# Kernel optimization log

Measured on AMD Instinct MI355X. Metric: run time of the kernel, lower is better.

The kernel has to match this reference:

```python
import jax, jax.numpy as jnp
import numpy as np

EPS = 1e-5

def _conv(x, w, b):
    # stride-2, pad-1 3x3 conv, NCHW / OIHW
    y = jax.lax.conv_general_dilated(x, w, (2, 2), [(1, 1), (1, 1)],
                                     dimension_numbers=('NCHW', 'OIHW', 'NCHW'))
    return y + b[None, :, None, None]

def _bn(x, gamma, beta):
    # training-mode batchnorm: batch statistics over (N,H,W), biased variance
    mu = x.mean(axis=(0, 2, 3), keepdims=True)
    var = x.var(axis=(0, 2, 3), keepdims=True)
    return gamma[None, :, None, None] * (x - mu) * jax.lax.rsqrt(var + EPS) + beta[None, :, None, None]

def setup_inputs():
    key = jax.random.key(0)
    ks = iter(jax.random.split(key, 40))
    def rn(shape, scale=0.05):
        return jax.random.normal(next(ks), shape, dtype=jnp.float32) * scale
    d = {}
    d['img'] = jax.random.normal(next(ks), (64, 3, 75, 75), dtype=jnp.float32)
    d['qst'] = jax.random.normal(next(ks), (64, 11), dtype=jnp.float32)
    # conv stack 3->32->64->128->256
    d['w1'] = rn((32, 3, 3, 3));    d['b1'] = jnp.zeros((32,), jnp.float32)
    d['w2'] = rn((64, 32, 3, 3));   d['b2'] = jnp.zeros((64,), jnp.float32)
    d['w3'] = rn((128, 64, 3, 3));  d['b3'] = jnp.zeros((128,), jnp.float32)
    d['w4'] = rn((256, 128, 3, 3)); d['b4'] = jnp.zeros((256,), jnp.float32)
    for i, c in zip((1, 2, 3, 4), (32, 64, 128, 256)):
        d[f'g{i}'] = jnp.ones((c,), jnp.float32)
        d[f'be{i}'] = jnp.zeros((c,), jnp.float32)
    # g MLP (torch Linear weights are [out,in])
    d['gw1'] = rn((2000, 523)); d['gb1'] = jnp.zeros((2000,), jnp.float32)
    d['gw2'] = rn((2000, 2000)); d['gb2'] = jnp.zeros((2000,), jnp.float32)
    d['gw3'] = rn((2000, 2000)); d['gb3'] = jnp.zeros((2000,), jnp.float32)
    d['gw4'] = rn((2000, 2000)); d['gb4'] = jnp.zeros((2000,), jnp.float32)
    # f MLP
    d['fw1'] = rn((1000, 2000)); d['fb1'] = jnp.zeros((1000,), jnp.float32)
    d['fw2'] = rn((500, 1000));  d['fb2'] = jnp.zeros((500,), jnp.float32)
    d['fw3'] = rn((100, 500));   d['fb3'] = jnp.zeros((100,), jnp.float32)
    d['fw4'] = rn((10, 100));    d['fb4'] = jnp.zeros((10,), jnp.float32)
    return d

def reference(img, qst, w1, b1, w2, b2, w3, b3, w4, b4,
              g1, be1, g2, be2, g3, be3, g4, be4,
              gw1, gb1, gw2, gb2, gw3, gb3, gw4, gb4,
              fw1, fb1, fw2, fb2, fw3, fb3, fw4, fb4):
    x = jax.nn.relu(_bn(_conv(img, w1, b1), g1, be1))
    x = jax.nn.relu(_bn(_conv(x, w2, b2), g2, be2))
    x = jax.nn.relu(_bn(_conv(x, w3, b3), g3, be3))
    x = jax.nn.relu(_bn(_conv(x, w4, b4), g4, be4))   # [B,256,5,5]
    B = x.shape[0]
    obj = x.reshape(B, 256, 25).transpose(0, 2, 1)     # [B,25,256], row-major like the loop
    oi = jnp.broadcast_to(obj[:, :, None, :], (B, 25, 25, 256))
    oj = jnp.broadcast_to(obj[:, None, :, :], (B, 25, 25, 256))
    q = jnp.broadcast_to(qst[:, None, None, :], (B, 25, 25, 11))
    pairs = jnp.concatenate([oi, oj, q], axis=-1).reshape(B * 625, 523)
    h = jax.nn.relu(pairs @ gw1.T + gb1)
    h = jax.nn.relu(h @ gw2.T + gb2)
    h = jax.nn.relu(h @ gw3.T + gb3)
    h = jax.nn.relu(h @ gw4.T + gb4)
    x_g = h.reshape(B, 625, 2000).sum(axis=1) / 625.0
    x_f = jax.nn.relu(x_g @ fw1.T + fb1)
    x_f = jax.nn.relu(x_f @ fw2.T + fb2)
    x_f = jax.nn.relu(x_f @ fw3.T + fb3)
    x_f = x_f @ fw4.T + fb4
    return jax.nn.log_softmax(x_f, axis=-1)
```

## Files before the change

### kernel.cpp

```cpp
#include <hip/hip_runtime.h>

typedef unsigned short u16;
typedef unsigned int u32;
typedef __attribute__((ext_vector_type(8))) short bf16x8;
typedef __attribute__((ext_vector_type(4))) float f32x4;

#define BN_EPS 1e-5f
#define BN_S 16

__device__ __forceinline__ float bf2f(u16 u) {
  union { unsigned u; float f; } x; x.u = ((unsigned)u) << 16; return x.f;
}
__device__ __forceinline__ u16 f2bf(float f) {
  union { float f; unsigned u; } x; x.f = f;
  unsigned r = x.u + 0x7FFFu + ((x.u >> 16) & 1u);
  return (u16)(r >> 16);
}

__global__ __launch_bounds__(256) void conv1_lds(const float* __restrict__ img,
                                                 const float* __restrict__ w,
                                                 const float* __restrict__ b,
                                                 float* __restrict__ C1) {
  int blk = blockIdx.x;
  int n = blk / 38, ho = blk % 38;
  __shared__ float in_s[9 * 80];
  __shared__ float w_s[32 * 27];
  __shared__ float b_s[32];
  int t = threadIdx.x;
  for (int i = t; i < 720; i += 256) in_s[i] = 0.f;
  __syncthreads();
  for (int i = t; i < 675; i += 256) {
    int wi = i % 75; int q = i / 75; int kh = q % 3; int ci = q / 3;
    int hi = ho * 2 - 1 + kh;
    if (hi >= 0 && hi < 75)
      in_s[(ci * 3 + kh) * 80 + wi + 1] = img[((size_t)(n * 3 + ci) * 75 + hi) * 75 + wi];
  }
  for (int i = t; i < 864; i += 256) w_s[i] = w[i];
  if (t < 32) b_s[t] = b[t];
  __syncthreads();
  for (int idx = t; idx < 1216; idx += 256) {
    int wo = idx >> 5, co = idx & 31;
    float acc = b_s[co];
    const float* wp = w_s + co * 27;
#pragma unroll
    for (int ci = 0; ci < 3; ci++) {
#pragma unroll
      for (int kh = 0; kh < 3; kh++) {
        const float* ip = in_s + (ci * 3 + kh) * 80 + 2 * wo;
        const float* wq = wp + ci * 9 + kh * 3;
        acc += ip[0] * wq[0] + ip[1] * wq[1] + ip[2] * wq[2];
      }
    }
    C1[((size_t)blk * 38 + wo) * 32 + co] = acc;
  }
}

__global__ void bn_partial(const float* __restrict__ C, int ldc, int M,
                           float* __restrict__ part) {
  int c = blockIdx.x; int s = blockIdx.y; int t = threadIdx.x;
  int rowsPer = (M + BN_S - 1) / BN_S;
  int r0 = s * rowsPer; int r1 = r0 + rowsPer; if (r1 > M) r1 = M;
  float s1 = 0.f, s2 = 0.f;
  for (int r = r0 + t; r < r1; r += 256) {
    float v = C[(size_t)r * ldc + c]; s1 += v; s2 += v * v;
  }
  __shared__ float l1[256], l2[256];
  l1[t] = s1; l2[t] = s2; __syncthreads();
  for (int off = 128; off > 0; off >>= 1) {
    if (t < off) { l1[t] += l1[t + off]; l2[t] += l2[t + off]; }
    __syncthreads();
  }
  if (t == 0) { part[s * 512 + c] = l1[0]; part[s * 512 + 256 + c] = l2[0]; }
}

__global__ void bn_final(const float* __restrict__ part, const float* __restrict__ gamma,
                         const float* __restrict__ beta, float* __restrict__ ss,
                         int C, int M) {
  int c = threadIdx.x;
  if (c >= C) { if (c < 256) { ss[c] = 0.f; ss[256 + c] = 0.f; } return; }
  float s1 = 0.f, s2 = 0.f;
#pragma unroll
  for (int s = 0; s < BN_S; s++) { s1 += part[s * 512 + c]; s2 += part[s * 512 + 256 + c]; }
  float mu = s1 / M;
  float var = s2 / M - mu * mu;
  float sc = gamma[c] * rsqrtf(var + BN_EPS);
  ss[c] = sc; ss[256 + c] = beta[c] - mu * sc;
}

__global__ void bnrelu_im2col(const float* __restrict__ Cprev, int ldprev, int Hp, int Wp,
                              const float* __restrict__ ss, u16* __restrict__ X,
                              int Ho, int Wo, int Ci, int Mp) {
  int civ4 = Ci >> 2;
  int idx = blockIdx.x * blockDim.x + threadIdx.x;
  int total = Mp * 9 * civ4;
  if (idx >= total) return;
  int cv = idx % civ4; int t2 = idx / civ4;
  int tap = t2 % 9; int row = t2 / 9;
  int K = 9 * Ci;
  u16* dst = X + (size_t)row * K + tap * Ci + cv * 4;
  int HW = Ho * Wo;
  int Mvalid = 64 * HW;
  ushort4 o4; o4.x = 0; o4.y = 0; o4.z = 0; o4.w = 0;
  if (row < Mvalid) {
    int wo = row % Wo; int t = row / Wo;
    int ho = t % Ho; int n = t / Ho;
    int kh = tap / 3, kw = tap % 3;
    int hi = ho * 2 - 1 + kh, wi = wo * 2 - 1 + kw;
    if (hi >= 0 && hi < Hp && wi >= 0 && wi < Wp) {
      const float* src = Cprev + ((size_t)((n * Hp + hi) * Wp + wi)) * ldprev + cv * 4;
      float4 v = *(const float4*)src;
      int c0 = cv * 4;
      float a;
      a = v.x * ss[c0 + 0] + ss[256 + c0 + 0]; o4.x = f2bf(a > 0.f ? a : 0.f);
      a = v.y * ss[c0 + 1] + ss[256 + c0 + 1]; o4.y = f2bf(a > 0.f ? a : 0.f);
      a = v.z * ss[c0 + 2] + ss[256 + c0 + 2]; o4.z = f2bf(a > 0.f ? a : 0.f);
      a = v.w * ss[c0 + 3] + ss[256 + c0 + 3]; o4.w = f2bf(a > 0.f ? a : 0.f);
    }
  }
  *(ushort4*)dst = o4;
}

__global__ void pack_convw(const float* __restrict__ w, u16* __restrict__ Wp,
                           int Co, int Ci, int Cop) {
  int K = 9 * Ci;
  int idx = blockIdx.x * blockDim.x + threadIdx.x;
  if (idx >= Cop * K) return;
  int k = idx % K; int co = idx / K;
  int tap = k / Ci; int ci = k % Ci;
  float v = (co < Co) ? w[((size_t)co * Ci + ci) * 9 + tap] : 0.f;
  Wp[idx] = f2bf(v);
}

__global__ void pad_bias(const float* __restrict__ b, float* __restrict__ bc, int Co, int Cop) {
  int i = blockIdx.x * blockDim.x + threadIdx.x;
  if (i < Cop) bc[i] = (i < Co) ? b[i] : 0.f;
}

__global__ void obj_from_c4(const float* __restrict__ C4, const float* __restrict__ ss,
                            u16* __restrict__ obj) {
  int idx = blockIdx.x * blockDim.x + threadIdx.x;
  if (idx >= 1664 * 256) return;
  int c = idx & 255; int row = idx >> 8;
  float v = 0.f;
  if (row < 1600) {
    float x = C4[(size_t)row * 256 + c];
    x = x * ss[c] + ss[256 + c];
    v = x > 0.f ? x : 0.f;
  }
  obj[idx] = f2bf(v);
}

__global__ void pack_w1(const float* __restrict__ gw1, u16* __restrict__ W1a, u16* __restrict__ W1b) {
  int idx = blockIdx.x * blockDim.x + threadIdx.x;
  if (idx >= 2048 * 256) return;
  int k = idx & 255, n = idx >> 8;
  float a = 0.f, b = 0.f;
  if (n < 2000) { a = gw1[(size_t)n * 523 + k]; b = gw1[(size_t)n * 523 + 256 + k]; }
  W1a[idx] = f2bf(a); W1b[idx] = f2bf(b);
}

__global__ void pack_wpad(const float* __restrict__ w, u16* __restrict__ Wp,
                          int N, int K, int Np, int Kp) {
  int idx = blockIdx.x * blockDim.x + threadIdx.x;
  if (idx >= Np * Kp) return;
  int k = idx % Kp, n = idx / Kp;
  float v = (n < N && k < K) ? w[(size_t)n * K + k] : 0.f;
  Wp[idx] = f2bf(v);
}

__global__ void pack_bias3(const float* __restrict__ b2, const float* __restrict__ b3,
                           const float* __restrict__ b4, float* __restrict__ bp) {
  int i = blockIdx.x * blockDim.x + threadIdx.x;
  if (i >= 2048) return;
  bp[i]        = (i < 2000) ? b2[i] : 0.f;
  bp[2048 + i] = (i < 2000) ? b3[i] : 0.f;
  bp[4096 + i] = (i < 2000) ? b4[i] : 0.f;
}

__global__ void q_build(const float* __restrict__ qst, const float* __restrict__ gw1,
                        const float* __restrict__ gb1, float* __restrict__ Q) {
  int idx = blockIdx.x * blockDim.x + threadIdx.x;
  if (idx >= 64 * 2048) return;
  int o = idx & 2047, b = idx >> 11;
  float v = 0.f;
  if (o < 2000) {
    v = gb1[o];
    const float* w = gw1 + (size_t)o * 523 + 512;
    const float* q = qst + b * 11;
#pragma unroll
    for (int k = 0; k < 11; k++) v += q[k] * w[k];
  }
  Q[idx] = v;
}

__global__ void pack_xgb(const float* __restrict__ xg, u16* __restrict__ xgb) {
  int idx = blockIdx.x * blockDim.x + threadIdx.x;
  if (idx >= 128 * 2048) return;
  int row = idx >> 11;
  float v = (row < 64) ? xg[idx] * (1.f / 625.f) : 0.f;
  xgb[idx] = f2bf(v);
}

typedef const __attribute__((address_space(1))) u32* gas1;
typedef __attribute__((address_space(3))) u32* las3;
__device__ __forceinline__ void gld16(const void* g, void* l) {
  __builtin_amdgcn_global_load_lds((gas1)g, (las3)l, 16, 0, 0);
}

template <int EPI>
__global__ __launch_bounds__(256) void gemm_bt(
    const u16* __restrict__ A, int lda,
    const u16* __restrict__ W, int ldb,
    float* __restrict__ Cf, u16* __restrict__ Cb, int ldc,
    const float* __restrict__ bias, int KT, int NTN) {
  __shared__ __align__(16) char lds[32768];
  int bid = blockIdx.x;
  int wg;
  if ((gridDim.x & 7) == 0) {
    int cpx = gridDim.x >> 3;
    wg = (bid & 7) * cpx + (bid >> 3);
  } else {
    wg = bid;
  }
  int mt = wg / NTN, nt = wg % NTN;
  int tid = threadIdx.x;
  int wave = tid >> 6, lane = tid & 63;
  int r = lane & 15, g = lane >> 4;
  int wr = wave >> 1, wc = wave & 1;

  const u16* Asrc = A + (size_t)(mt * 128 + wave * 32 + r) * lda + g * 8;
  const u16* Wsrc = W + (size_t)(nt * 128 + wave * 32 + r) * ldb + g * 8;

  f32x4 acc[4][4];
#pragma unroll
  for (int i = 0; i < 4; i++)
#pragma unroll
    for (int j = 0; j < 4; j++) acc[i][j] = (f32x4){0.f, 0.f, 0.f, 0.f};

  {
    char* Al = lds; char* Wl = lds + 8192;
    gld16(Asrc, Al + wave * 2048);
    gld16(Asrc + (size_t)16 * lda, Al + wave * 2048 + 1024);
    gld16(Wsrc, Wl + wave * 2048);
    gld16(Wsrc + (size_t)16 * ldb, Wl + wave * 2048 + 1024);
  }
  __syncthreads();

  int buf = 0;
  for (int kt = 0; kt < KT; kt++) {
    if (kt + 1 < KT) {
      int k0 = (kt + 1) * 32;
      char* Al = lds + (buf ^ 1) * 16384; char* Wl = Al + 8192;
      gld16(Asrc + k0, Al + wave * 2048);
      gld16(Asrc + k0 + (size_t)16 * lda, Al + wave * 2048 + 1024);
      gld16(Wsrc + k0, Wl + wave * 2048);
      gld16(Wsrc + k0 + (size_t)16 * ldb, Wl + wave * 2048 + 1024);
    }
    char* Al = lds + buf * 16384; char* Wl = Al + 8192;
    bf16x8 a[4], w[4];
#pragma unroll
    for (int i = 0; i < 4; i++) a[i] = *(const bf16x8*)(Al + (wr * 4 + i) * 1024 + lane * 16);
#pragma unroll
    for (int j = 0; j < 4; j++) w[j] = *(const bf16x8*)(Wl + (wc * 4 + j) * 1024 + lane * 16);
#pragma unroll
    for (int i = 0; i < 4; i++)
#pragma unroll
      for (int j = 0; j < 4; j++)
        acc[i][j] = __builtin_amdgcn_mfma_f32_16x16x32_bf16(a[i], w[j], acc[i][j], 0, 0, 0);
    __syncthreads();
    buf ^= 1;
  }

  int rowb = mt * 128 + wr * 64 + (lane >> 4) * 4;
  int colb = nt * 128 + wc * 64 + (lane & 15);
#pragma unroll
  for (int i = 0; i < 4; i++) {
#pragma unroll
    for (int j = 0; j < 4; j++) {
      int col = colb + j * 16;
      float bv = (EPI == 2 || EPI == 5) ? bias[col] : 0.f;
#pragma unroll
      for (int q = 0; q < 4; q++) {
        int row = rowb + i * 16 + q;
        float v = acc[i][j][q];
        if (EPI == 2) {
          Cf[(size_t)row * ldc + col] = v + bv;
        } else if (EPI == 3) {
          Cb[(size_t)row * ldc + col] = f2bf(v);
        } else if (EPI == 5) {
          float z = v + bv; z = z > 0.f ? z : 0.f;
          Cb[(size_t)row * ldc + col] = f2bf(z);
        } else {
          Cf[(size_t)row * ldc + col] = v;
        }
      }
    }
  }
}

#define MF16(d, av, bv) d = __builtin_amdgcn_mfma_f32_16x16x32_bf16(av, bv, d, 0, 0, 0)

template <int NT, int SUM>
__global__ __launch_bounds__(512, 2) void gemm256(
    const u16* __restrict__ A, const u16* __restrict__ W,
    u16* __restrict__ Cb, const float* __restrict__ bias,
    float* __restrict__ rp4, int r0c, int nvalid) {
  __shared__ __align__(16) char lds[131072];
  int bid = blockIdx.x;
  int cpx = gridDim.x >> 3;
  int wg = (bid & 7) * cpx + (bid >> 3);
  int mt = wg >> 3, nt = wg & 7;
  int tid = threadIdx.x;
  int wave = tid >> 6, lane = tid & 63;
  int wr = wave >> 2, wc = wave & 3;
  int wcl = wc & 1, wch = wc >> 1;
  int l15 = lane & 15, l7 = lane & 7, lh = lane >> 4;

  int srcChunkOff = (((lane & 7) ^ (lane >> 3)) << 3);
  int srcRowInWave = (lane >> 3);
  auto stageA = [&](int tt, int slot, int h) {
#pragma unroll
    for (int s = 0; s < 2; s++) {
      const u16* src = A + (size_t)(mt * 256 + h * 128 + s * 64 + wave * 8 + srcRowInWave) * 2048
                         + tt * 64 + srcChunkOff;
      gld16(src, lds + slot * 65536 + h * 16384 + s * 8192 + wave * 1024);
    }
  };
  auto stageB = [&](int tt, int slot, int h) {
#pragma unroll
    for (int s = 0; s < 2; s++) {
      const u16* src = W + (size_t)(nt * 256 + h * 128 + s * 64 + wave * 8 + srcRowInWave) * 2048
                         + tt * 64 + srcChunkOff;
      gld16(src, lds + slot * 65536 + 32768 + h * 16384 + s * 8192 + wave * 1024);
    }
  };

  f32x4 acc[8][4];
#pragma unroll
  for (int i = 0; i < 8; i++)
#pragma unroll
    for (int j = 0; j < 4; j++) acc[i][j] = (f32x4){0.f, 0.f, 0.f, 0.f};

  stageA(0, 0, 0); stageA(0, 0, 1); stageB(0, 0, 0); stageB(0, 0, 1);
  stageB(1, 1, 0); stageB(1, 1, 1);
  asm volatile("s_waitcnt vmcnt(4)" ::: "memory");
  __builtin_amdgcn_s_barrier();

  bf16x8 b00, b01, b10, b11, b20, b21, b30, b31;

#define AROFF(Q, i, ks) \
  ((((2 * (Q) + (i)) * 16 + l15) * 128) + (((((ks) * 4) + lh) ^ l7) << 4))
#define BROFF(j, ks) \
  ((((wcl * 4 + (j)) * 16 + l15) * 128) + (((((ks) * 4) + lh) ^ l7) << 4))

#define PHASE(Q, T, BUF)                                                         \
  {                                                                              \
    const char* Ab = lds + (BUF) * 65536 + wr * 16384;                           \
    const char* Bb = lds + (BUF) * 65536 + 32768 + wch * 16384;                  \
    if (Q == 0) {                                                                \
      b00 = *(const bf16x8*)(Bb + BROFF(0, 0));                                  \
      b01 = *(const bf16x8*)(Bb + BROFF(0, 1));                                  \
      b10 = *(const bf16x8*)(Bb + BROFF(1, 0));                                  \
      b11 = *(const bf16x8*)(Bb + BROFF(1, 1));                                  \
      b20 = *(const bf16x8*)(Bb + BROFF(2, 0));                                  \
      b21 = *(const bf16x8*)(Bb + BROFF(2, 1));                                  \
      b30 = *(const bf16x8*)(Bb + BROFF(3, 0));                                  \
      b31 = *(const bf16x8*)(Bb + BROFF(3, 1));                                  \
    }                                                                            \
    bf16x8 a00 = *(const bf16x8*)(Ab + AROFF(Q, 0, 0));                          \
    bf16x8 a01 = *(const bf16x8*)(Ab + AROFF(Q, 0, 1));                          \
    bf16x8 a10 = *(const bf16x8*)(Ab + AROFF(Q, 1, 0));                          \
    bf16x8 a11 = *(const bf16x8*)(Ab + AROFF(Q, 1, 1));                          \
    if (Q == 0) { if ((T) + 1 < NT) stageA((T) + 1, (BUF) ^ 1, 0); }             \
    if (Q == 1) { if ((T) + 1 < NT) stageA((T) + 1, (BUF) ^ 1, 1);               \
                  if ((T) + 2 < NT) stageB((T) + 2, (BUF), 0); }                 \
    if (Q == 2) { if ((T) + 2 < NT) stageB((T) + 2, (BUF), 1); }                 \
    __builtin_amdgcn_s_barrier();                                                \
    __builtin_amdgcn_s_setprio(1);                                               \
    MF16(acc[2 * Q + 0][0], a00, b00); MF16(acc[2 * Q + 0][0], a01, b01);        \
    MF16(acc[2 * Q + 0][1], a00, b10); MF16(acc[2 * Q + 0][1], a01, b11);        \
    MF16(acc[2 * Q + 0][2], a00, b20); MF16(acc[2 * Q + 0][2], a01, b21);        \
    MF16(acc[2 * Q + 0][3], a00, b30); MF16(acc[2 * Q + 0][3], a01, b31);        \
    MF16(acc[2 * Q + 1][0], a10, b00); MF16(acc[2 * Q + 1][0], a11, b01);        \
    MF16(acc[2 * Q + 1][1], a10, b10); MF16(acc[2 * Q + 1][1], a11, b11);        \
    MF16(acc[2 * Q + 1][2], a10, b20); MF16(acc[2 * Q + 1][2], a11, b21);        \
    MF16(acc[2 * Q + 1][3], a10, b30); MF16(acc[2 * Q + 1][3], a11, b31);        \
    __builtin_amdgcn_s_setprio(0);                                               \
    if (Q == 3) { asm volatile("s_waitcnt vmcnt(4)" ::: "memory"); }             \
    __builtin_amdgcn_s_barrier();                                                \
  }

#pragma unroll 1
  for (int t2 = 0; t2 < NT; t2 += 2) {
    PHASE(0, t2, 0) PHASE(1, t2, 0) PHASE(2, t2, 0) PHASE(3, t2, 0)
    PHASE(0, t2 + 1, 1) PHASE(1, t2 + 1, 1) PHASE(2, t2 + 1, 1) PHASE(3, t2 + 1, 1)
  }
#undef PHASE
#undef AROFF
#undef BROFF

  int colb = nt * 256 + wc * 64 + l15;
  if (SUM == 0) {
    int rowb = mt * 256 + wr * 128 + lh * 4;
#pragma unroll
    for (int i = 0; i < 8; i++) {
#pragma unroll
      for (int j = 0; j < 4; j++) {
        int col = colb + j * 16;
        float bv = bias[col];
#pragma unroll
        for (int q = 0; q < 4; q++) {
          int row = rowb + i * 16 + q;
          float v = acc[i][j][q] + bv;
          v = v > 0.f ? v : 0.f;
          Cb[(size_t)row * 2048 + col] = f2bf(v);
        }
      }
    }
  } else {
    int blockRow0 = mt * 256;
    int bimg = (r0c + blockRow0) / 625;
    int boundary = (bimg + 1) * 625 - (r0c + blockRow0);
    float p0[4] = {0.f, 0.f, 0.f, 0.f};
    float p1[4] = {0.f, 0.f, 0.f, 0.f};
#pragma unroll
    for (int i = 0; i < 8; i++) {
#pragma unroll
      for (int j = 0; j < 4; j++) {
        float bv = bias[colb + j * 16];
#pragma unroll
        for (int q = 0; q < 4; q++) {
          int row_local = wr * 128 + lh * 4 + i * 16 + q;
          float v = acc[i][j][q] + bv;
          v = v > 0.f ? v : 0.f;
          if (blockRow0 + row_local >= nvalid) v = 0.f;
          bool sg1 = row_local >= boundary;
          p0[j] += sg1 ? 0.f : v;
          p1[j] += sg1 ? v : 0.f;
        }
      }
    }
    float* rs = (float*)lds;
    int contrib = wr * 4 + lh;
#pragma unroll
    for (int j = 0; j < 4; j++) {
      int colL = wc * 64 + j * 16 + l15;
      rs[(contrib * 2 + 0) * 256 + colL] = p0[j];
      rs[(contrib * 2 + 1) * 256 + colL] = p1[j];
    }
    __syncthreads();
    int seg = tid >> 8, colx = tid & 255;
    float s = 0.f;
#pragma unroll
    for (int c8 = 0; c8 < 8; c8++) s += rs[(c8 * 2 + seg) * 256 + colx];
    rp4[((size_t)(mt * 2 + seg)) * 2048 + nt * 256 + colx] = s;
  }
}

__global__ void h1_build(const u16* __restrict__ Af, const u16* __restrict__ Bf,
                         const float* __restrict__ Q, u16* __restrict__ h1,
                         int r0, int nvalid) {
  int lrow = blockIdx.x;
  int t = threadIdx.x;
  u16* dst = h1 + (size_t)lrow * 2048;
  if (lrow >= nvalid) {
#pragma unroll
    for (int it = 0; it < 2; it++) {
      int o = it * 1024 + t * 4;
      ushort4 z; z.x = 0; z.y = 0; z.z = 0; z.w = 0;
      *(ushort4*)(dst + o) = z;
    }
    return;
  }
  int grow = r0 + lrow;
  int b = grow / 625; int rem = grow % 625;
  int i = rem / 25, j = rem % 25;
  const u16* Ap = Af + (size_t)(b * 25 + i) * 2048;
  const u16* Bp = Bf + (size_t)(b * 25 + j) * 2048;
  const float* Qp = Q + (size_t)b * 2048;
#pragma unroll
  for (int it = 0; it < 2; it++) {
    int o = it * 1024 + t * 4;
    ushort4 a4 = *(const ushort4*)(Ap + o);
    ushort4 b4 = *(const ushort4*)(Bp + o);
    float4 qv = *(const float4*)(Qp + o);
    ushort4 outv;
    float v;
    v = bf2f(a4.x) + bf2f(b4.x) + qv.x; outv.x = f2bf(v > 0.f ? v : 0.f);
    v = bf2f(a4.y) + bf2f(b4.y) + qv.y; outv.y = f2bf(v > 0.f ? v : 0.f);
    v = bf2f(a4.z) + bf2f(b4.z) + qv.z; outv.z = f2bf(v > 0.f ? v : 0.f);
    v = bf2f(a4.w) + bf2f(b4.w) + qv.w; outv.w = f2bf(v > 0.f ? v : 0.f);
    *(ushort4*)(dst + o) = outv;
  }
}

__global__ void zero_xg(float* __restrict__ xg) {
  int i = blockIdx.x * blockDim.x + threadIdx.x;
  if (i < 64 * 2048) xg[i] = 0.f;
}

__global__ void l4_fin(const float* __restrict__ rp4, float* __restrict__ xg,
                       int r0, int bfirst, int mtiles) {
  int col = blockIdx.x * 256 + threadIdx.x;
  int b = bfirst + blockIdx.y;
  if (b > 63) return;
  float s = 0.f;
  for (int mt = 0; mt < mtiles; mt++) {
    int img0 = (r0 + mt * 256) / 625;
    if (img0 == b)     s += rp4[((size_t)(mt * 2 + 0)) * 2048 + col];
    if (img0 + 1 == b) s += rp4[((size_t)(mt * 2 + 1)) * 2048 + col];
  }
  xg[(size_t)b * 2048 + col] += s;
}

__global__ void f_layer4(const u16* __restrict__ x, const float* __restrict__ Wf,
                         const float* __restrict__ bf_, float* __restrict__ y) {
  int gwid = (blockIdx.x * blockDim.x + threadIdx.x) >> 6;
  int lane = threadIdx.x & 63;
  if (gwid >= 64 * 10) return;
  int b = gwid / 10, o = gwid % 10;
  const u16* xp = x + (size_t)b * 128;
  const float* wp = Wf + (size_t)o * 100;
  float s = 0.f;
  for (int k = lane; k < 100; k += 64) s += bf2f(xp[k]) * wp[k];
  for (int off = 32; off > 0; off >>= 1) s += __shfl_down(s, off);
  if (lane == 0) y[b * 16 + o] = s + bf_[o];
}

__global__ void lsm_kernel(const float* __restrict__ xf4, float* __restrict__ out) {
  int b = blockIdx.x * blockDim.x + threadIdx.x;
  if (b >= 64) return;
  const float* x = xf4 + b * 16;
  float m = x[0];
  for (int i = 1; i < 10; i++) m = fmaxf(m, x[i]);
  float s = 0.f;
  for (int i = 0; i < 10; i++) s += expf(x[i] - m);
  float ls = logf(s);
  for (int i = 0; i < 10; i++) out[b * 10 + i] = x[i] - m - ls;
}

extern "C" void kernel_launch(void* const* d_in, const int* in_sizes, int n_in,
                              void* d_out, int out_size, void* d_ws, size_t ws_size,
                              hipStream_t stream) {
  const float* img = (const float*)d_in[0];
  const float* qst = (const float*)d_in[1];
  const float* w1 = (const float*)d_in[2];  const float* b1 = (const float*)d_in[3];
  const float* w2 = (const float*)d_in[4];  const float* b2 = (const float*)d_in[5];
  const float* w3 = (const float*)d_in[6];  const float* b3 = (const float*)d_in[7];
  const float* w4 = (const float*)d_in[8];  const float* b4 = (const float*)d_in[9];
  const float* g1 = (const float*)d_in[10]; const float* be1 = (const float*)d_in[11];
  const float* g2 = (const float*)d_in[12]; const float* be2 = (const float*)d_in[13];
  const float* g3 = (const float*)d_in[14]; const float* be3 = (const float*)d_in[15];
  const float* g4 = (const float*)d_in[16]; const float* be4 = (const float*)d_in[17];
  const float* gw1 = (const float*)d_in[18]; const float* gb1 = (const float*)d_in[19];
  const float* gw2 = (const float*)d_in[20]; const float* gb2 = (const float*)d_in[21];
  const float* gw3 = (const float*)d_in[22]; const float* gb3 = (const float*)d_in[23];
  const float* gw4 = (const float*)d_in[24]; const float* gb4 = (const float*)d_in[25];
  const float* fw1 = (const float*)d_in[26]; const float* fb1 = (const float*)d_in[27];
  const float* fw2 = (const float*)d_in[28]; const float* fb2 = (const float*)d_in[29];
  const float* fw3 = (const float*)d_in[30]; const float* fb3 = (const float*)d_in[31];
  const float* fw4 = (const float*)d_in[32]; const float* fb4 = (const float*)d_in[33];
  float* out = (float*)d_out;

  char* P = (char*)d_ws;
  auto alloc = [&](size_t bytes) -> char* {
    char* r = P; P += (bytes + 255) & ~(size_t)255; return r;
  };
  u16* Wp2 = (u16*)alloc(2048ull * 2048 * 2);
  u16* Wp3 = (u16*)alloc(2048ull * 2048 * 2);
  u16* Wp4 = (u16*)alloc(2048ull * 2048 * 2);
  u16* Afu = (u16*)alloc(1664ull * 2048 * 2);
  u16* Bfu = (u16*)alloc(1664ull * 2048 * 2);
  float* Q = (float*)alloc(64ull * 2048 * 4);
  float* bp = (float*)alloc(3ull * 2048 * 4);
  float* xg = (float*)alloc(64ull * 2048 * 4);
  u16* obj = (u16*)alloc(1664ull * 256 * 2);
  u16* W1a = (u16*)alloc(2048ull * 256 * 2);
  u16* W1b = (u16*)alloc(2048ull * 256 * 2);
  float* rp4 = (float*)alloc(160ull * 2 * 2048 * 4);
  u16* Fp1 = (u16*)alloc(1024ull * 2048 * 2);
  u16* Fp2 = (u16*)alloc(512ull * 1024 * 2);
  u16* Fp3 = (u16*)alloc(128ull * 512 * 2);
  float* fbc1 = (float*)alloc(1024 * 4);
  float* fbc2 = (float*)alloc(512 * 4);
  float* fbc3 = (float*)alloc(128 * 4);
  u16* xgb  = (u16*)alloc(128ull * 2048 * 2);
  u16* xf1b = (u16*)alloc(128ull * 1024 * 2);
  u16* xf2b = (u16*)alloc(128ull * 512 * 2);
  u16* xf3b = (u16*)alloc(128ull * 128 * 2);
  float* xf4 = (float*)alloc(64ull * 16 * 4);
  float* C1 = (float*)alloc(92416ull * 32 * 4);
  u16*   X2 = (u16*)alloc(23168ull * 288 * 2);
  float* C2 = (float*)alloc(23168ull * 128 * 4);
  u16*   X3 = (u16*)alloc(6400ull * 576 * 2);
  float* C3 = (float*)alloc(6400ull * 128 * 4);
  u16*   X4 = (u16*)alloc(1664ull * 1152 * 2);
  float* C4 = (float*)alloc(1664ull * 256 * 4);
  u16*  Wc2 = (u16*)alloc(128ull * 288 * 2);
  u16*  Wc3 = (u16*)alloc(128ull * 576 * 2);
  u16*  Wc4 = (u16*)alloc(256ull * 1152 * 2);
  float* bc2 = (float*)alloc(128 * 4);
  float* bc3 = (float*)alloc(128 * 4);
  float* bc4 = (float*)alloc(256 * 4);
  float* bnp = (float*)alloc(BN_S * 512 * 4);
  float* ss  = (float*)alloc(512 * 4);

  size_t used = (size_t)(P - (char*)d_ws);
  size_t remain = (ws_size > used) ? (ws_size - used) : 0;
  int CHMAX;
  if (remain >= 2ull * 40960 * 2048 * 2 + 4096)      CHMAX = 40960;
  else if (remain >= 2ull * 16384 * 2048 * 2 + 4096) CHMAX = 16384;
  else                                               CHMAX = 8192;
  u16* h0  = (u16*)alloc((size_t)CHMAX * 2048 * 2);
  u16* h1b = (u16*)alloc((size_t)CHMAX * 2048 * 2);

  pack_convw<<<(128 * 288 + 255) / 256, 256, 0, stream>>>(w2, Wc2, 64, 32, 128);
  pack_convw<<<(128 * 576 + 255) / 256, 256, 0, stream>>>(w3, Wc3, 128, 64, 128);
  pack_convw<<<(256 * 1152 + 255) / 256, 256, 0, stream>>>(w4, Wc4, 256, 128, 256);
  pad_bias<<<1, 256, 0, stream>>>(b2, bc2, 64, 128);
  pad_bias<<<1, 256, 0, stream>>>(b3, bc3, 128, 128);
  pad_bias<<<1, 256, 0, stream>>>(b4, bc4, 256, 256);

  conv1_lds<<<64 * 38, 256, 0, stream>>>(img, w1, b1, C1);
  bn_partial<<<dim3(32, BN_S), 256, 0, stream>>>(C1, 32, 92416, bnp);
  bn_final<<<1, 256, 0, stream>>>(bnp, g1, be1, ss, 32, 92416);
  bnrelu_im2col<<<(23168 * 9 * 8 + 255) / 256, 256, 0, stream>>>(C1, 32, 38, 38, ss, X2, 19, 19, 32, 23168);
  gemm_bt<2><<<181, 256, 0, stream>>>(X2, 288, Wc2, 288, C2, nullptr, 128, bc2, 9, 1);

  bn_partial<<<dim3(64, BN_S), 256, 0, stream>>>(C2, 128, 23104, bnp);
  bn_final<<<1, 256, 0, stream>>>(bnp, g2, be2, ss, 64, 23104);
  bnrelu_im2col<<<(6400 * 9 * 16 + 255) / 256, 256, 0, stream>>>(C2, 128, 19, 19, ss, X3, 10, 10, 64, 6400);
  gemm_bt<2><<<50, 256, 0, stream>>>(X3, 576, Wc3, 576, C3, nullptr, 128, bc3, 18, 1);

  bn_partial<<<dim3(128, BN_S), 256, 0, stream>>>(C3, 128, 6400, bnp);
  bn_final<<<1, 256, 0, stream>>>(bnp, g3, be3, ss, 128, 6400);
  bnrelu_im2col<<<(1664 * 9 * 32 + 255) / 256, 256, 0, stream>>>(C3, 128, 10, 10, ss, X4, 5, 5, 128, 1664);
  gemm_bt<2><<<26, 256, 0, stream>>>(X4, 1152, Wc4, 1152, C4, nullptr, 256, bc4, 36, 2);

  bn_partial<<<dim3(256, BN_S), 256, 0, stream>>>(C4, 256, 1600, bnp);
  bn_final<<<1, 256, 0, stream>>>(bnp, g4, be4, ss, 256, 1600);
  obj_from_c4<<<(1664 * 256 + 255) / 256, 256, 0, stream>>>(C4, ss, obj);

  pack_w1<<<2048, 256, 0, stream>>>(gw1, W1a, W1b);
  pack_wpad<<<(2048 * 2048 + 255) / 256, 256, 0, stream>>>(gw2, Wp2, 2000, 2000, 2048, 2048);
  pack_wpad<<<(2048 * 2048 + 255) / 256, 256, 0, stream>>>(gw3, Wp3, 2000, 2000, 2048, 2048);
  pack_wpad<<<(2048 * 2048 + 255) / 256, 256, 0, stream>>>(gw4, Wp4, 2000, 2000, 2048, 2048);
  pack_bias3<<<8, 256, 0, stream>>>(gb2, gb3, gb4, bp);
  q_build<<<512, 256, 0, stream>>>(qst, gw1, gb1, Q);
  pack_wpad<<<(1024 * 2048 + 255) / 256, 256, 0, stream>>>(fw1, Fp1, 1000, 2000, 1024, 2048);
  pack_wpad<<<(512 * 1024 + 255) / 256, 256, 0, stream>>>(fw2, Fp2, 500, 1000, 512, 1024);
  pack_wpad<<<(128 * 512 + 255) / 256, 256, 0, stream>>>(fw3, Fp3, 100, 500, 128, 512);
  pad_bias<<<4, 256, 0, stream>>>(fb1, fbc1, 1000, 1024);
  pad_bias<<<2, 256, 0, stream>>>(fb2, fbc2, 500, 512);
  pad_bias<<<1, 256, 0, stream>>>(fb3, fbc3, 100, 128);

  gemm_bt<3><<<13 * 16, 256, 0, stream>>>(obj, 256, W1a, 256, nullptr, Afu, 2048, nullptr, 8, 16);
  gemm_bt<3><<<13 * 16, 256, 0, stream>>>(obj, 256, W1b, 256, nullptr, Bfu, 2048, nullptr, 8, 16);

  zero_xg<<<512, 256, 0, stream>>>(xg);
  const int TOTPAD = 40960;
  const int TOTROWS = 40000;
  int r0 = 0;
  while (r0 < TOTPAD) {
    int CH = (TOTPAD - r0 >= CHMAX) ? CHMAX : (TOTPAD - r0);
    int nvalid = TOTROWS - r0; if (nvalid > CH) nvalid = CH; if (nvalid < 0) nvalid = 0;
    int mtiles = CH / 256;
    h1_build<<<(unsigned)CH, 256, 0, stream>>>(Afu, Bfu, Q, h0, r0, nvalid);
    gemm256<32, 0><<<mtiles * 8, 512, 0, stream>>>(h0, Wp2, h1b, bp, nullptr, 0, 0);
    gemm256<32, 0><<<mtiles * 8, 512, 0, stream>>>(h1b, Wp3, h0, bp + 2048, nullptr, 0, 0);
    gemm256<32, 1><<<mtiles * 8, 512, 0, stream>>>(h0, Wp4, nullptr, bp + 4096, rp4, r0, nvalid);
    int bfirst = r0 / 625;
    int blast = (r0 + CH - 1) / 625; if (blast > 63) blast = 63;
    int nseg = blast - bfirst + 1;
    l4_fin<<<dim3(8, nseg), 256, 0, stream>>>(rp4, xg, r0, bfirst, mtiles);
    r0 += CH;
  }

  pack_xgb<<<(128 * 2048 + 255) / 256, 256, 0, stream>>>(xg, xgb);
  gemm_bt<5><<<8, 256, 0, stream>>>(xgb, 2048, Fp1, 2048, nullptr, xf1b, 1024, fbc1, 64, 8);
  gemm_bt<5><<<4, 256, 0, stream>>>(xf1b, 1024, Fp2, 1024, nullptr, xf2b, 512, fbc2, 32, 4);
  gemm_bt<5><<<1, 256, 0, stream>>>(xf2b, 512, Fp3, 512, nullptr, xf3b, 128, fbc3, 16, 1);
  f_layer4<<<(64 * 10 * 64 + 255) / 256, 256, 0, stream>>>(xf3b, fw4, fb4, xf4);
  lsm_kernel<<<1, 64, 0, stream>>>(xf4, out);
}
```

Baseline: 1.200 ms.

## Software-pipeline LDS fragment loads one phase ahead of MFMA in GEMM

```diff
diff --git a/kernel.cpp b/kernel.cpp
--- a/kernel.cpp
+++ b/kernel.cpp
@@ -346,47 +346,73 @@
   asm volatile("s_waitcnt vmcnt(4)" ::: "memory");
   __builtin_amdgcn_s_barrier();
 
-  bf16x8 b00, b01, b10, b11, b20, b21, b30, b31;
-
 #define AROFF(Q, i, ks) \
   ((((2 * (Q) + (i)) * 16 + l15) * 128) + (((((ks) * 4) + lh) ^ l7) << 4))
 #define BROFF(j, ks) \
   ((((wcl * 4 + (j)) * 16 + l15) * 128) + (((((ks) * 4) + lh) ^ l7) << 4))
 
+  bf16x8 a00, a01, a10, a11;
+  bf16x8 b00, b01, b10, b11, b20, b21, b30, b31;
+  {
+    const char* Ab0 = lds + wr * 16384;
+    const char* Bb0 = lds + 32768 + wch * 16384;
+    a00 = *(const bf16x8*)(Ab0 + AROFF(0, 0, 0));
+    a01 = *(const bf16x8*)(Ab0 + AROFF(0, 0, 1));
+    a10 = *(const bf16x8*)(Ab0 + AROFF(0, 1, 0));
+    a11 = *(const bf16x8*)(Ab0 + AROFF(0, 1, 1));
+    b00 = *(const bf16x8*)(Bb0 + BROFF(0, 0));
+    b01 = *(const bf16x8*)(Bb0 + BROFF(0, 1));
+    b10 = *(const bf16x8*)(Bb0 + BROFF(1, 0));
+    b11 = *(const bf16x8*)(Bb0 + BROFF(1, 1));
+    b20 = *(const bf16x8*)(Bb0 + BROFF(2, 0));
+    b21 = *(const bf16x8*)(Bb0 + BROFF(2, 1));
+    b30 = *(const bf16x8*)(Bb0 + BROFF(3, 0));
+    b31 = *(const bf16x8*)(Bb0 + BROFF(3, 1));
+  }
+
 #define PHASE(Q, T, BUF)                                                         \
   {                                                                              \
-    const char* Ab = lds + (BUF) * 65536 + wr * 16384;                           \
-    const char* Bb = lds + (BUF) * 65536 + 32768 + wch * 16384;                  \
-    if (Q == 0) {                                                                \
-      b00 = *(const bf16x8*)(Bb + BROFF(0, 0));                                  \
-      b01 = *(const bf16x8*)(Bb + BROFF(0, 1));                                  \
-      b10 = *(const bf16x8*)(Bb + BROFF(1, 0));                                  \
-      b11 = *(const bf16x8*)(Bb + BROFF(1, 1));                                  \
-      b20 = *(const bf16x8*)(Bb + BROFF(2, 0));                                  \
-      b21 = *(const bf16x8*)(Bb + BROFF(2, 1));                                  \
-      b30 = *(const bf16x8*)(Bb + BROFF(3, 0));                                  \
-      b31 = *(const bf16x8*)(Bb + BROFF(3, 1));                                  \
-    }                                                                            \
-    bf16x8 a00 = *(const bf16x8*)(Ab + AROFF(Q, 0, 0));                          \
-    bf16x8 a01 = *(const bf16x8*)(Ab + AROFF(Q, 0, 1));                          \
-    bf16x8 a10 = *(const bf16x8*)(Ab + AROFF(Q, 1, 0));                          \
-    bf16x8 a11 = *(const bf16x8*)(Ab + AROFF(Q, 1, 1));                          \
-    if (Q == 0) { if ((T) + 1 < NT) stageA((T) + 1, (BUF) ^ 1, 0); }             \
-    if (Q == 1) { if ((T) + 1 < NT) stageA((T) + 1, (BUF) ^ 1, 1);               \
-                  if ((T) + 2 < NT) stageB((T) + 2, (BUF), 0); }                 \
-    if (Q == 2) { if ((T) + 2 < NT) stageB((T) + 2, (BUF), 1); }                 \
+    if ((Q) == 0) { if ((T) + 1 < NT) stageA((T) + 1, (BUF) ^ 1, 0); }           \
+    if ((Q) == 1) { if ((T) + 1 < NT) stageA((T) + 1, (BUF) ^ 1, 1);             \
+                    if ((T) + 2 < NT) stageB((T) + 2, (BUF), 0); }               \
+    if ((Q) == 2) { if ((T) + 2 < NT) stageB((T) + 2, (BUF), 1); }               \
     __builtin_amdgcn_s_barrier();                                                \
     __builtin_amdgcn_s_setprio(1);                                               \
-    MF16(acc[2 * Q + 0][0], a00, b00); MF16(acc[2 * Q + 0][0], a01, b01);        \
-    MF16(acc[2 * Q + 0][1], a00, b10); MF16(acc[2 * Q + 0][1], a01, b11);        \
-    MF16(acc[2 * Q + 0][2], a00, b20); MF16(acc[2 * Q + 0][2], a01, b21);        \
-    MF16(acc[2 * Q + 0][3], a00, b30); MF16(acc[2 * Q + 0][3], a01, b31);        \
-    MF16(acc[2 * Q + 1][0], a10, b00); MF16(acc[2 * Q + 1][0], a11, b01);        \
-    MF16(acc[2 * Q + 1][1], a10, b10); MF16(acc[2 * Q + 1][1], a11, b11);        \
-    MF16(acc[2 * Q + 1][2], a10, b20); MF16(acc[2 * Q + 1][2], a11, b21);        \
-    MF16(acc[2 * Q + 1][3], a10, b30); MF16(acc[2 * Q + 1][3], a11, b31);        \
+    MF16(acc[2 * (Q) + 0][0], a00, b00); MF16(acc[2 * (Q) + 0][0], a01, b01);    \
+    MF16(acc[2 * (Q) + 0][1], a00, b10); MF16(acc[2 * (Q) + 0][1], a01, b11);    \
+    MF16(acc[2 * (Q) + 0][2], a00, b20); MF16(acc[2 * (Q) + 0][2], a01, b21);    \
+    MF16(acc[2 * (Q) + 0][3], a00, b30); MF16(acc[2 * (Q) + 0][3], a01, b31);    \
+    MF16(acc[2 * (Q) + 1][0], a10, b00); MF16(acc[2 * (Q) + 1][0], a11, b01);    \
+    MF16(acc[2 * (Q) + 1][1], a10, b10); MF16(acc[2 * (Q) + 1][1], a11, b11);    \
+    MF16(acc[2 * (Q) + 1][2], a10, b20); MF16(acc[2 * (Q) + 1][2], a11, b21);    \
+    MF16(acc[2 * (Q) + 1][3], a10, b30); MF16(acc[2 * (Q) + 1][3], a11, b31);    \
     __builtin_amdgcn_s_setprio(0);                                               \
-    if (Q == 3) { asm volatile("s_waitcnt vmcnt(4)" ::: "memory"); }             \
+    if ((Q) < 3) {                                                               \
+      const char* Ab_ = lds + (BUF) * 65536 + wr * 16384;                        \
+      a00 = *(const bf16x8*)(Ab_ + AROFF((Q) + 1, 0, 0));                        \
+      a01 = *(const bf16x8*)(Ab_ + AROFF((Q) + 1, 0, 1));                        \
+      a10 = *(const bf16x8*)(Ab_ + AROFF((Q) + 1, 1, 0));                        \
+      a11 = *(const bf16x8*)(Ab_ + AROFF((Q) + 1, 1, 1));                        \
+    } else if ((T) + 1 < NT) {                                                   \
+      const char* AbN_ = lds + (((BUF) ^ 1)) * 65536 + wr * 16384;               \
+      const char* BbN_ = lds + (((BUF) ^ 1)) * 65536 + 32768 + wch * 16384;      \
+      a00 = *(const bf16x8*)(AbN_ + AROFF(0, 0, 0));                             \
+      a01 = *(const bf16x8*)(AbN_ + AROFF(0, 0, 1));                             \
+      a10 = *(const bf16x8*)(AbN_ + AROFF(0, 1, 0));                             \
+      a11 = *(const bf16x8*)(AbN_ + AROFF(0, 1, 1));                             \
+      b00 = *(const bf16x8*)(BbN_ + BROFF(0, 0));                                \
+      b01 = *(const bf16x8*)(BbN_ + BROFF(0, 1));                                \
+      b10 = *(const bf16x8*)(BbN_ + BROFF(1, 0));                                \
+      b11 = *(const bf16x8*)(BbN_ + BROFF(1, 1));                                \
+      b20 = *(const bf16x8*)(BbN_ + BROFF(2, 0));                                \
+      b21 = *(const bf16x8*)(BbN_ + BROFF(2, 1));                                \
+      b30 = *(const bf16x8*)(BbN_ + BROFF(3, 0));                                \
+      b31 = *(const bf16x8*)(BbN_ + BROFF(3, 1));                                \
+    }                                                                            \
+    if ((Q) == 2) {                                                              \
+      if ((T) + 2 < NT) { asm volatile("s_waitcnt vmcnt(4)" ::: "memory"); }     \
+      else              { asm volatile("s_waitcnt vmcnt(0)" ::: "memory"); }     \
+    }                                                                            \
     __builtin_amdgcn_s_barrier();                                                \
   }
 
@@ -609,6 +635,7 @@
   size_t remain = (ws_size > used) ? (ws_size - used) : 0;
   int CHMAX;
   if (remain >= 2ull * 40960 * 2048 * 2 + 4096)      CHMAX = 40960;
+  else if (remain >= 2ull * 24576 * 2048 * 2 + 4096) CHMAX = 24576;
   else if (remain >= 2ull * 16384 * 2048 * 2 + 4096) CHMAX = 16384;
   else                                               CHMAX = 8192;
   u16* h0  = (u16*)alloc((size_t)CHMAX * 2048 * 2);
```

Result: no change. 1.191 ms (median of 3 runs) (-0.8%).

## Replace 256x256 g-MLP GEMM with 256x128 tile, smaller K-step, higher occupancy

Applied to the files above, without the earlier changes.

```diff
diff --git a/kernel.cpp b/kernel.cpp
--- a/kernel.cpp
+++ b/kernel.cpp
@@ -301,109 +301,80 @@
 #define MF16(d, av, bv) d = __builtin_amdgcn_mfma_f32_16x16x32_bf16(av, bv, d, 0, 0, 0)
 
 template <int NT, int SUM>
-__global__ __launch_bounds__(512, 2) void gemm256(
+__global__ __launch_bounds__(512, 4) void gemm128(
     const u16* __restrict__ A, const u16* __restrict__ W,
     u16* __restrict__ Cb, const float* __restrict__ bias,
     float* __restrict__ rp4, int r0c, int nvalid) {
-  __shared__ __align__(16) char lds[131072];
+  __shared__ __align__(16) char lds[49152];
   int bid = blockIdx.x;
   int cpx = gridDim.x >> 3;
   int wg = (bid & 7) * cpx + (bid >> 3);
-  int mt = wg >> 3, nt = wg & 7;
+  int mt = wg >> 4, nt = wg & 15;
   int tid = threadIdx.x;
   int wave = tid >> 6, lane = tid & 63;
-  int wr = wave >> 2, wc = wave & 3;
-  int wcl = wc & 1, wch = wc >> 1;
-  int l15 = lane & 15, l7 = lane & 7, lh = lane >> 4;
-
-  int srcChunkOff = (((lane & 7) ^ (lane >> 3)) << 3);
-  int srcRowInWave = (lane >> 3);
-  auto stageA = [&](int tt, int slot, int h) {
+  int wr = wave >> 1, wc = wave & 1;
+  int l15 = lane & 15, lh = lane >> 4;
+
+  int srcChunkElems = (((tid & 3) ^ ((tid >> 3) & 3)) << 3);
+  int rowInSweep = (tid >> 2);
+  auto stage = [&](int tt, int slot) {
 #pragma unroll
     for (int s = 0; s < 2; s++) {
-      const u16* src = A + (size_t)(mt * 256 + h * 128 + s * 64 + wave * 8 + srcRowInWave) * 2048
-                         + tt * 64 + srcChunkOff;
-      gld16(src, lds + slot * 65536 + h * 16384 + s * 8192 + wave * 1024);
+      const u16* src = A + (size_t)(mt * 256 + s * 128 + rowInSweep) * 2048
+                         + tt * 32 + srcChunkElems;
+      gld16(src, lds + slot * 24576 + s * 8192 + wave * 1024);
+    }
+    {
+      const u16* src = W + (size_t)(nt * 128 + rowInSweep) * 2048
+                         + tt * 32 + srcChunkElems;
+      gld16(src, lds + slot * 24576 + 16384 + wave * 1024);
     }
   };
-  auto stageB = [&](int tt, int slot, int h) {
-#pragma unroll
-    for (int s = 0; s < 2; s++) {
-      const u16* src = W + (size_t)(nt * 256 + h * 128 + s * 64 + wave * 8 + srcRowInWave) * 2048
-                         + tt * 64 + srcChunkOff;
-      gld16(src, lds + slot * 65536 + 32768 + h * 16384 + s * 8192 + wave * 1024);
-    }
-  };
-
-  f32x4 acc[8][4];
-#pragma unroll
-  for (int i = 0; i < 8; i++)
+
+  f32x4 acc[4][4];
+#pragma unroll
+  for (int i = 0; i < 4; i++)
 #pragma unroll
     for (int j = 0; j < 4; j++) acc[i][j] = (f32x4){0.f, 0.f, 0.f, 0.f};
 
-  stageA(0, 0, 0); stageA(0, 0, 1); stageB(0, 0, 0); stageB(0, 0, 1);
-  stageB(1, 1, 0); stageB(1, 1, 1);
-  asm volatile("s_waitcnt vmcnt(4)" ::: "memory");
+  stage(0, 0);
+  asm volatile("s_waitcnt vmcnt(0)" ::: "memory");
   __builtin_amdgcn_s_barrier();
 
-  bf16x8 b00, b01, b10, b11, b20, b21, b30, b31;
-
-#define AROFF(Q, i, ks) \
-  ((((2 * (Q) + (i)) * 16 + l15) * 128) + (((((ks) * 4) + lh) ^ l7) << 4))
-#define BROFF(j, ks) \
-  ((((wcl * 4 + (j)) * 16 + l15) * 128) + (((((ks) * 4) + lh) ^ l7) << 4))
-
-#define PHASE(Q, T, BUF)                                                         \
-  {                                                                              \
-    const char* Ab = lds + (BUF) * 65536 + wr * 16384;                           \
-    const char* Bb = lds + (BUF) * 65536 + 32768 + wch * 16384;                  \
-    if (Q == 0) {                                                                \
-      b00 = *(const bf16x8*)(Bb + BROFF(0, 0));                                  \
-      b01 = *(const bf16x8*)(Bb + BROFF(0, 1));                                  \
-      b10 = *(const bf16x8*)(Bb + BROFF(1, 0));                                  \
-      b11 = *(const bf16x8*)(Bb + BROFF(1, 1));                                  \
-      b20 = *(const bf16x8*)(Bb + BROFF(2, 0));                                  \
-      b21 = *(const bf16x8*)(Bb + BROFF(2, 1));                                  \
-      b30 = *(const bf16x8*)(Bb + BROFF(3, 0));                                  \
-      b31 = *(const bf16x8*)(Bb + BROFF(3, 1));                                  \
-    }                                                                            \
-    bf16x8 a00 = *(const bf16x8*)(Ab + AROFF(Q, 0, 0));                          \
-    bf16x8 a01 = *(const bf16x8*)(Ab + AROFF(Q, 0, 1));                          \
-    bf16x8 a10 = *(const bf16x8*)(Ab + AROFF(Q, 1, 0));                          \
-    bf16x8 a11 = *(const bf16x8*)(Ab + AROFF(Q, 1, 1));                          \
-    if (Q == 0) { if ((T) + 1 < NT) stageA((T) + 1, (BUF) ^ 1, 0); }             \
-    if (Q == 1) { if ((T) + 1 < NT) stageA((T) + 1, (BUF) ^ 1, 1);               \
-                  if ((T) + 2 < NT) stageB((T) + 2, (BUF), 0); }                 \
-    if (Q == 2) { if ((T) + 2 < NT) stageB((T) + 2, (BUF), 1); }                 \
-    __builtin_amdgcn_s_barrier();                                                \
-    __builtin_amdgcn_s_setprio(1);                                               \
-    MF16(acc[2 * Q + 0][0], a00, b00); MF16(acc[2 * Q + 0][0], a01, b01);        \
-    MF16(acc[2 * Q + 0][1], a00, b10); MF16(acc[2 * Q + 0][1], a01, b11);        \
-    MF16(acc[2 * Q + 0][2], a00, b20); MF16(acc[2 * Q + 0][2], a01, b21);        \
-    MF16(acc[2 * Q + 0][3], a00, b30); MF16(acc[2 * Q + 0][3], a01, b31);        \
-    MF16(acc[2 * Q + 1][0], a10, b00); MF16(acc[2 * Q + 1][0], a11, b01);        \
-    MF16(acc[2 * Q + 1][1], a10, b10); MF16(acc[2 * Q + 1][1], a11, b11);        \
-    MF16(acc[2 * Q + 1][2], a10, b20); MF16(acc[2 * Q + 1][2], a11, b21);        \
-    MF16(acc[2 * Q + 1][3], a10, b30); MF16(acc[2 * Q + 1][3], a11, b31);        \
-    __builtin_amdgcn_s_setprio(0);                                               \
-    if (Q == 3) { asm volatile("s_waitcnt vmcnt(4)" ::: "memory"); }             \
-    __builtin_amdgcn_s_barrier();                                                \
-  }
+  int rdChunk = ((lh ^ ((l15 >> 1) & 3)) << 4);
 
 #pragma unroll 1
-  for (int t2 = 0; t2 < NT; t2 += 2) {
-    PHASE(0, t2, 0) PHASE(1, t2, 0) PHASE(2, t2, 0) PHASE(3, t2, 0)
-    PHASE(0, t2 + 1, 1) PHASE(1, t2 + 1, 1) PHASE(2, t2 + 1, 1) PHASE(3, t2 + 1, 1)
-  }
-#undef PHASE
-#undef AROFF
-#undef BROFF
-
-  int colb = nt * 256 + wc * 64 + l15;
+  for (int t = 0; t < NT; t++) {
+    int slot = t & 1;
+    if (t + 1 < NT) stage(t + 1, slot ^ 1);
+    const char* base = lds + slot * 24576;
+    bf16x8 a0 = *(const bf16x8*)(base + (wr * 64 + 0 * 16 + l15) * 64 + rdChunk);
+    bf16x8 a1 = *(const bf16x8*)(base + (wr * 64 + 1 * 16 + l15) * 64 + rdChunk);
+    bf16x8 a2 = *(const bf16x8*)(base + (wr * 64 + 2 * 16 + l15) * 64 + rdChunk);
+    bf16x8 a3 = *(const bf16x8*)(base + (wr * 64 + 3 * 16 + l15) * 64 + rdChunk);
+    bf16x8 b0 = *(const bf16x8*)(base + 16384 + (wc * 64 + 0 * 16 + l15) * 64 + rdChunk);
+    bf16x8 b1 = *(const bf16x8*)(base + 16384 + (wc * 64 + 1 * 16 + l15) * 64 + rdChunk);
+    bf16x8 b2 = *(const bf16x8*)(base + 16384 + (wc * 64 + 2 * 16 + l15) * 64 + rdChunk);
+    bf16x8 b3 = *(const bf16x8*)(base + 16384 + (wc * 64 + 3 * 16 + l15) * 64 + rdChunk);
+    __builtin_amdgcn_s_setprio(1);
+    MF16(acc[0][0], a0, b0); MF16(acc[0][1], a0, b1);
+    MF16(acc[0][2], a0, b2); MF16(acc[0][3], a0, b3);
+    MF16(acc[1][0], a1, b0); MF16(acc[1][1], a1, b1);
+    MF16(acc[1][2], a1, b2); MF16(acc[1][3], a1, b3);
+    MF16(acc[2][0], a2, b0); MF16(acc[2][1], a2, b1);
+    MF16(acc[2][2], a2, b2); MF16(acc[2][3], a2, b3);
+    MF16(acc[3][0], a3, b0); MF16(acc[3][1], a3, b1);
+    MF16(acc[3][2], a3, b2); MF16(acc[3][3], a3, b3);
+    __builtin_amdgcn_s_setprio(0);
+    asm volatile("s_waitcnt vmcnt(0)" ::: "memory");
+    __builtin_amdgcn_s_barrier();
+  }
+
+  int colb = nt * 128 + wc * 64 + l15;
   if (SUM == 0) {
-    int rowb = mt * 256 + wr * 128 + lh * 4;
-#pragma unroll
-    for (int i = 0; i < 8; i++) {
+    int rowb = mt * 256 + wr * 64 + lh * 4;
+#pragma unroll
+    for (int i = 0; i < 4; i++) {
 #pragma unroll
       for (int j = 0; j < 4; j++) {
         int col = colb + j * 16;
@@ -424,13 +395,13 @@
     float p0[4] = {0.f, 0.f, 0.f, 0.f};
     float p1[4] = {0.f, 0.f, 0.f, 0.f};
 #pragma unroll
-    for (int i = 0; i < 8; i++) {
+    for (int i = 0; i < 4; i++) {
 #pragma unroll
       for (int j = 0; j < 4; j++) {
         float bv = bias[colb + j * 16];
 #pragma unroll
         for (int q = 0; q < 4; q++) {
-          int row_local = wr * 128 + lh * 4 + i * 16 + q;
+          int row_local = wr * 64 + lh * 4 + i * 16 + q;
           float v = acc[i][j][q] + bv;
           v = v > 0.f ? v : 0.f;
           if (blockRow0 + row_local >= nvalid) v = 0.f;
@@ -445,15 +416,17 @@
 #pragma unroll
     for (int j = 0; j < 4; j++) {
       int colL = wc * 64 + j * 16 + l15;
-      rs[(contrib * 2 + 0) * 256 + colL] = p0[j];
-      rs[(contrib * 2 + 1) * 256 + colL] = p1[j];
+      rs[(contrib * 2 + 0) * 128 + colL] = p0[j];
+      rs[(contrib * 2 + 1) * 128 + colL] = p1[j];
     }
     __syncthreads();
-    int seg = tid >> 8, colx = tid & 255;
-    float s = 0.f;
-#pragma unroll
-    for (int c8 = 0; c8 < 8; c8++) s += rs[(c8 * 2 + seg) * 256 + colx];
-    rp4[((size_t)(mt * 2 + seg)) * 2048 + nt * 256 + colx] = s;
+    if (tid < 256) {
+      int seg = tid >> 7, colx = tid & 127;
+      float s = 0.f;
+#pragma unroll
+      for (int c16 = 0; c16 < 16; c16++) s += rs[(c16 * 2 + seg) * 128 + colx];
+      rp4[((size_t)(mt * 2 + seg)) * 2048 + nt * 128 + colx] = s;
+    }
   }
 }
 
@@ -609,6 +582,7 @@
   size_t remain = (ws_size > used) ? (ws_size - used) : 0;
   int CHMAX;
   if (remain >= 2ull * 40960 * 2048 * 2 + 4096)      CHMAX = 40960;
+  else if (remain >= 2ull * 24576 * 2048 * 2 + 4096) CHMAX = 24576;
   else if (remain >= 2ull * 16384 * 2048 * 2 + 4096) CHMAX = 16384;
   else                                               CHMAX = 8192;
   u16* h0  = (u16*)alloc((size_t)CHMAX * 2048 * 2);
@@ -666,9 +640,9 @@
     int nvalid = TOTROWS - r0; if (nvalid > CH) nvalid = CH; if (nvalid < 0) nvalid = 0;
     int mtiles = CH / 256;
     h1_build<<<(unsigned)CH, 256, 0, stream>>>(Afu, Bfu, Q, h0, r0, nvalid);
-    gemm256<32, 0><<<mtiles * 8, 512, 0, stream>>>(h0, Wp2, h1b, bp, nullptr, 0, 0);
-    gemm256<32, 0><<<mtiles * 8, 512, 0, stream>>>(h1b, Wp3, h0, bp + 2048, nullptr, 0, 0);
-    gemm256<32, 1><<<mtiles * 8, 512, 0, stream>>>(h0, Wp4, nullptr, bp + 4096, rp4, r0, nvalid);
+    gemm128<64, 0><<<mtiles * 16, 512, 0, stream>>>(h0, Wp2, h1b, bp, nullptr, 0, 0);
+    gemm128<64, 0><<<mtiles * 16, 512, 0, stream>>>(h1b, Wp3, h0, bp + 2048, nullptr, 0, 0);
+    gemm128<64, 1><<<mtiles * 16, 512, 0, stream>>>(h0, Wp4, nullptr, bp + 4096, rp4, r0, nvalid);
     int bfirst = r0 / 625;
     int blast = (r0 + CH - 1) / 625; if (blast > 63) blast = 63;
     int nseg = blast - bfirst + 1;
```

New measurement: 1.324 ms. 1.1x slower.
